# Optimization experiments

Measured on AMD Instinct MI355X. Metric: run time of the kernel, lower is better.

Reference implementation:

```python
import jax, jax.numpy as jnp
import numpy as np

B, N, D, H = 2, 2048, 128, 128  # batch, n_nodes, node_dim, hidden_dim
HQ = H // 4
EPS_DIST = 1e-8
EPS_LN = 1e-5


def setup_inputs() -> dict:
    key = jax.random.key(0)
    ks = jax.random.split(key, 12)
    s = 0.02
    return {
        "h": jax.random.normal(ks[0], (B, N, D), jnp.float32),
        "coords": jax.random.uniform(ks[1], (B, N, 2), jnp.float32),
        "Wq": jax.random.normal(ks[2], (D, H), jnp.float32) * s,
        "bq": jnp.zeros((H,), jnp.float32),
        "Wk": jax.random.normal(ks[3], (D, H), jnp.float32) * s,
        "bk": jnp.zeros((H,), jnp.float32),
        "Wv": jax.random.normal(ks[4], (D, H), jnp.float32) * s,
        "bv": jnp.zeros((H,), jnp.float32),
        "Wd1": jax.random.normal(ks[5], (1, HQ), jnp.float32) * s,
        "bd1": jnp.zeros((HQ,), jnp.float32),
        "Wd2": jax.random.normal(ks[6], (HQ, 1), jnp.float32) * s,
        "bd2": jnp.zeros((1,), jnp.float32),
        "Wo": jax.random.normal(ks[7], (H, D), jnp.float32) * s,
        "bo": jnp.zeros((D,), jnp.float32),
        "gamma": jnp.ones((D,), jnp.float32),
        "beta": jnp.zeros((D,), jnp.float32),
    }


def reference(h, coords, Wq, bq, Wk, bk, Wv, bv, Wd1, bd1, Wd2, bd2, Wo, bo, gamma, beta):
    q = h @ Wq + bq                      # (B, N, H)
    k = h @ Wk + bk
    v = h @ Wv + bv
    scores = jnp.einsum('bnh,bmh->bnm', q, k) / jnp.sqrt(jnp.float32(H))  # (B,N,N)
    # pairwise Euclidean distances
    diff = coords[:, :, None, :] - coords[:, None, :, :]                  # (B,N,N,2)
    dist = jnp.sqrt(jnp.sum(diff * diff, axis=-1, keepdims=True) + EPS_DIST)  # (B,N,N,1)
    hmid = jax.nn.silu(dist @ Wd1 + bd1)                                  # (B,N,N,HQ)
    dist_bias = (hmid @ Wd2 + bd2)[..., 0]                                # (B,N,N)
    attn = jax.nn.softmax(scores + dist_bias, axis=-1)
    out = jnp.einsum('bnm,bmh->bnh', attn, v)                             # (B,N,H)
    out = jax.nn.silu(out @ Wo + bo)                                      # (B,N,D)
    res = h + out
    mu = jnp.mean(res, axis=-1, keepdims=True)
    var = jnp.mean((res - mu) ** 2, axis=-1, keepdims=True)
    return (res - mu) / jnp.sqrt(var + EPS_LN) * gamma + beta
```

## Files before the change

### kernel.cpp

```cpp
#include <hip/hip_runtime.h>
#include <hip/hip_bf16.h>

#define B_ 2
#define N_ 2048
#define D_ 128
#define H_ 128
#define HQ_ 32
#define ROWS_ (B_*N_)
#define KS_ 16
#define KPP_ (N_/KS_)
#define DMAX_ 1.4143f
#define SCALE_ 0.08838834764831845f
#define LOG2E_ 1.4426950408889634f

typedef __bf16 bf16x4 __attribute__((ext_vector_type(4)));
typedef __bf16 bf16x8 __attribute__((ext_vector_type(8)));
typedef float  f32x4  __attribute__((ext_vector_type(4)));
typedef unsigned short ushort8 __attribute__((ext_vector_type(8)));

#if __has_builtin(__builtin_amdgcn_exp2f)
#define EXP2F_ __builtin_amdgcn_exp2f
#else
#define EXP2F_ exp2f
#endif
#if __has_builtin(__builtin_amdgcn_sqrtf)
#define SQRTF_ __builtin_amdgcn_sqrtf
#else
#define SQRTF_ sqrtf
#endif

#define Q_OFF    0
#define K_OFF    (ROWS_*H_*2)
#define V_OFF    (2*ROWS_*H_*2)
#define L_OFF    (3*ROWS_*H_*2)
#define OP_OFF   (L_OFF + ROWS_*KS_*4)
#define HB_OFF   (OP_OFF + (size_t)ROWS_*KS_*H_*2)
#define WT_OFF   (HB_OFF + ROWS_*D_*2)
#define CF_OFF   (WT_OFF + 3*D_*H_*2)

__global__ __launch_bounds__(256) void prep_kernel(
    const float* __restrict__ h,
    const float* __restrict__ Wq, const float* __restrict__ Wk, const float* __restrict__ Wv,
    const float* __restrict__ Wd1, const float* __restrict__ bd1,
    const float* __restrict__ Wd2, const float* __restrict__ bd2,
    __bf16* __restrict__ hb, __bf16* __restrict__ Wt, float* __restrict__ cf)
{
    const int bid = blockIdx.x, t = threadIdx.x;
    if (bid < 256) {
        const float4* src = (const float4*)(h + (size_t)bid * 2048);
        __bf16* dst = hb + (size_t)bid * 2048;
        #pragma unroll
        for (int i = 0; i < 2; ++i) {
            float4 v = src[t + i * 256];
            bf16x4 pk = { (__bf16)v.x, (__bf16)v.y, (__bf16)v.z, (__bf16)v.w };
            *(bf16x4*)(dst + (t + i * 256) * 4) = pk;
        }
    } else if (bid < 280) {
        __shared__ float tile[128][17];
        const int id = bid - 256;
        const int m = id >> 3, ch = id & 7;
        const float* W = m == 0 ? Wq : (m == 1 ? Wk : Wv);
        const int c0 = ch * 16;
        #pragma unroll
        for (int i = 0; i < 8; ++i) {
            int idx = t + i * 256;
            int k = idx >> 4, cc = idx & 15;
            tile[k][cc] = W[k * 128 + c0 + cc];
        }
        __syncthreads();
        __bf16* dst = Wt + m * 16384;
        #pragma unroll
        for (int i = 0; i < 8; ++i) {
            int idx = t + i * 256;
            int cc = idx >> 7, k = idx & 127;
            dst[(c0 + cc) * 128 + k] = (__bf16)tile[k][cc];
        }
    } else if (t < 64) {
        const int j = t & 31;
        const float w1 = Wd1[j], b1 = bd1[j];
        const float w2h = Wd2[j] * 0.5f;
        float gv[5];
        #pragma unroll
        for (int i = 0; i < 5; ++i) {
            float d = (DMAX_ * 0.25f) * (float)i;
            float x = fmaf(d, w1, b1);
            gv[i] = (x / (1.f + __expf(-x))) * w2h;
        }
        #pragma unroll
        for (int i = 0; i < 5; ++i)
            #pragma unroll
            for (int off = 1; off < 64; off <<= 1) gv[i] += __shfl_xor(gv[i], off);
        if (t == 0) {
            const float bd2v = bd2[0];
            float g0 = (gv[0] + bd2v) * LOG2E_, g1 = (gv[1] + bd2v) * LOG2E_,
                  g2 = (gv[2] + bd2v) * LOG2E_, g3 = (gv[3] + bd2v) * LOG2E_,
                  g4 = (gv[4] + bd2v) * LOG2E_;
            cf[0] = g0;
            cf[1] = -2.0833333333f*g0 + 4.f*g1 - 3.f*g2 + 1.3333333333f*g3 - 0.25f*g4;
            cf[2] =  1.4583333333f*g0 - 4.3333333333f*g1 + 4.75f*g2 - 2.3333333333f*g3 + 0.4583333333f*g4;
            cf[3] = -0.4166666667f*g0 + 1.5f*g1 - 2.f*g2 + 1.1666666667f*g3 - 0.25f*g4;
            cf[4] =  0.0416666667f*g0 - 0.1666666667f*g1 + 0.25f*g2 - 0.1666666667f*g3 + 0.0416666667f*g4;
        }
    }
}

__global__ __launch_bounds__(256) void qkv_mfma(
    const __bf16* __restrict__ hb, const __bf16* __restrict__ Wt,
    const float* __restrict__ bq, const float* __restrict__ bk, const float* __restrict__ bv,
    __bf16* __restrict__ qb, __bf16* __restrict__ kb, __bf16* __restrict__ vb)
{
    const int t = threadIdx.x, wid = t >> 6, lane = t & 63;
    const int l16 = lane & 15, g = lane >> 4;
    const int row0 = blockIdx.x * 64 + wid * 16;
    const int co   = blockIdx.y * 32;
    const int which = co >> 7, c0 = co & 127;
    const __bf16* Wm = Wt + which * 16384;
    __bf16* outp      = which == 0 ? qb : (which == 1 ? kb : vb);
    const float* bias = which == 0 ? bq : (which == 1 ? bk : bv);
    const float scale = which == 0 ? (SCALE_ * LOG2E_) : 1.f;

    bf16x8 af[4];
    const __bf16* arow = hb + (size_t)(row0 + l16) * 128;
    #pragma unroll
    for (int kk = 0; kk < 4; ++kk) af[kk] = *(const bf16x8*)(arow + kk * 32 + g * 8);

    f32x4 acc0 = {0.f,0.f,0.f,0.f}, acc1 = {0.f,0.f,0.f,0.f};
    const __bf16* b0 = Wm + (size_t)(c0 + l16) * 128;
    const __bf16* b1 = Wm + (size_t)(c0 + 16 + l16) * 128;
    #pragma unroll
    for (int kk = 0; kk < 4; ++kk) {
        bf16x8 f0 = *(const bf16x8*)(b0 + kk * 32 + g * 8);
        acc0 = __builtin_amdgcn_mfma_f32_16x16x32_bf16(af[kk], f0, acc0, 0, 0, 0);
    }
    #pragma unroll
    for (int kk = 0; kk < 4; ++kk) {
        bf16x8 f1 = *(const bf16x8*)(b1 + kk * 32 + g * 8);
        acc1 = __builtin_amdgcn_mfma_f32_16x16x32_bf16(af[kk], f1, acc1, 0, 0, 0);
    }
    const float bv0 = bias[c0 + l16], bv1 = bias[c0 + 16 + l16];
    #pragma unroll
    for (int i = 0; i < 4; ++i) {
        size_t r = (size_t)(row0 + g * 4 + i) * 128;
        outp[r + c0 + l16]      = (__bf16)((acc0[i] + bv0) * scale);
        outp[r + c0 + 16 + l16] = (__bf16)((acc1[i] + bv1) * scale);
    }
}

__global__ __launch_bounds__(256, 3) void attn_kernel(
    const __bf16* __restrict__ qb, const __bf16* __restrict__ kb, const __bf16* __restrict__ vb,
    const float* __restrict__ coords, const float* __restrict__ cfp,
    unsigned int* __restrict__ Opb32, float* __restrict__ Larr)
{
    __shared__ __align__(16) unsigned int Vsu[2][128][20];
    __shared__ __align__(16) __bf16 Pl[4][2][16][40];

    const int t    = threadIdx.x;
    const int wid  = t >> 6;
    const int lane = t & 63;
    const int l16  = lane & 15;
    const int g    = lane >> 4;
    const int qb0  = blockIdx.x * 128 + wid * 16;
    const int p    = blockIdx.y;
    const int b    = blockIdx.x >> 4;

    const float c0 = cfp[0], c1 = cfp[1], c2 = cfp[2], c3 = cfp[3], c4 = cfp[4];

    bf16x8 qf[2][4];
    #pragma unroll
    for (int tt = 0; tt < 2; ++tt) {
        const __bf16* qrow = qb + (size_t)(qb0 + tt * 64 + l16) * H_;
        #pragma unroll
        for (int kk = 0; kk < 4; ++kk) qf[tt][kk] = *(const bf16x8*)(qrow + kk * 32 + g * 8);
    }

    float cx[2][4], cy[2][4];
    #pragma unroll
    for (int tt = 0; tt < 2; ++tt)
        #pragma unroll
        for (int i = 0; i < 4; ++i) {
            int qr = qb0 + tt * 64 + g * 4 + i;
            cx[tt][i] = coords[qr * 2]; cy[tt][i] = coords[qr * 2 + 1];
        }

    float l_i[2][4] = {{0.f,0.f,0.f,0.f},{0.f,0.f,0.f,0.f}};
    f32x4 O0[8], O1[8];
    #pragma unroll
    for (int c = 0; c < 8; ++c) { O0[c] = (f32x4){0.f,0.f,0.f,0.f}; O1[c] = (f32x4){0.f,0.f,0.f,0.f}; }

    const int kp = t & 15, co = t >> 4;
    const int kgbase = (b << 11) + p * KPP_;
    const int NT = KPP_ / 32;

    {
        const __bf16* sp = vb + (size_t)(kgbase + 2 * kp) * H_ + co * 8;
        bf16x8 va = *(const bf16x8*)sp;
        bf16x8 vb2 = *(const bf16x8*)(sp + H_);
        ushort8 ua = __builtin_bit_cast(ushort8, va);
        ushort8 ub = __builtin_bit_cast(ushort8, vb2);
        #pragma unroll
        for (int j = 0; j < 8; ++j)
            Vsu[0][co * 8 + j][kp] = (unsigned)ua[j] | ((unsigned)ub[j] << 16);
    }

    for (int kt = 0; kt < NT; ++kt) {
        __syncthreads();

        bf16x8 nva, nvb;
        if (kt + 1 < NT) {
            const __bf16* sp = vb + (size_t)(kgbase + (kt + 1) * 32 + 2 * kp) * H_ + co * 8;
            nva = *(const bf16x8*)sp;
            nvb = *(const bf16x8*)(sp + H_);
        }

        const int kg = kgbase + kt * 32;
        #pragma unroll
        for (int mt = 0; mt < 2; ++mt) {
            bf16x8 kf[4];
            const __bf16* krow = kb + (size_t)(kg + mt * 16 + l16) * H_;
            #pragma unroll
            for (int kk = 0; kk < 4; ++kk) kf[kk] = *(const bf16x8*)(krow + kk * 32 + g * 8);

            f32x4 acc0 = {0.f,0.f,0.f,0.f}, acc1 = {0.f,0.f,0.f,0.f};
            #pragma unroll
            for (int kk = 0; kk < 4; ++kk)
                acc0 = __builtin_amdgcn_mfma_f32_16x16x32_bf16(qf[0][kk], kf[kk], acc0, 0, 0, 0);
            #pragma unroll
            for (int kk = 0; kk < 4; ++kk)
                acc1 = __builtin_amdgcn_mfma_f32_16x16x32_bf16(qf[1][kk], kf[kk], acc1, 0, 0, 0);

            float2 kc = *(const float2*)&coords[(kg + mt * 16 + l16) * 2];
            #pragma unroll
            for (int i = 0; i < 4; ++i) {
                float dx = cx[0][i] - kc.x, dy = cy[0][i] - kc.y;
                float dist = SQRTF_(fmaf(dx, dx, fmaf(dy, dy, 1e-8f)));
                float s4 = dist * (4.0f / DMAX_);
                float bias = fmaf(fmaf(fmaf(fmaf(c4, s4, c3), s4, c2), s4, c1), s4, c0);
                float sc = fminf(acc0[i] + bias, 80.f);
                float pe = EXP2F_(sc);
                l_i[0][i] += pe;
                Pl[wid][0][g * 4 + i][mt * 16 + l16] = (__bf16)pe;
            }
            #pragma unroll
            for (int i = 0; i < 4; ++i) {
                float dx = cx[1][i] - kc.x, dy = cy[1][i] - kc.y;
                float dist = SQRTF_(fmaf(dx, dx, fmaf(dy, dy, 1e-8f)));
                float s4 = dist * (4.0f / DMAX_);
                float bias = fmaf(fmaf(fmaf(fmaf(c4, s4, c3), s4, c2), s4, c1), s4, c0);
                float sc = fminf(acc1[i] + bias, 80.f);
                float pe = EXP2F_(sc);
                l_i[1][i] += pe;
                Pl[wid][1][g * 4 + i][mt * 16 + l16] = (__bf16)pe;
            }
        }

        if (kt + 1 < NT) {
            ushort8 ua = __builtin_bit_cast(ushort8, nva);
            ushort8 ub = __builtin_bit_cast(ushort8, nvb);
            #pragma unroll
            for (int j = 0; j < 8; ++j)
                Vsu[(kt + 1) & 1][co * 8 + j][kp] = (unsigned)ua[j] | ((unsigned)ub[j] << 16);
        }

        bf16x8 pf0 = *(const bf16x8*)&Pl[wid][0][l16][g * 8];
        bf16x8 pf1 = *(const bf16x8*)&Pl[wid][1][l16][g * 8];
        #pragma unroll
        for (int c = 0; c < 8; ++c) {
            bf16x8 vf = *(const bf16x8*)&Vsu[kt & 1][c * 16 + l16][g * 4];
            O0[c] = __builtin_amdgcn_mfma_f32_16x16x32_bf16(pf0, vf, O0[c], 0, 0, 0);
            O1[c] = __builtin_amdgcn_mfma_f32_16x16x32_bf16(pf1, vf, O1[c], 0, 0, 0);
        }
    }

    #pragma unroll
    for (int tt = 0; tt < 2; ++tt) {
        const size_t rpbase = (size_t)p * (ROWS_ / 2) + ((qb0 + tt * 64) >> 1) + g * 2;
        #pragma unroll
        for (int c = 0; c < 8; ++c)
            #pragma unroll
            for (int ip = 0; ip < 2; ++ip) {
                float lo_f = tt ? O1[c][2 * ip]     : O0[c][2 * ip];
                float hi_f = tt ? O1[c][2 * ip + 1] : O0[c][2 * ip + 1];
                unsigned lo = __builtin_bit_cast(unsigned, lo_f);
                unsigned hi = __builtin_bit_cast(unsigned, hi_f);
                Opb32[(rpbase + ip) * H_ + c * 16 + l16] = (hi & 0xffff0000u) | (lo >> 16);
            }
    }

    #pragma unroll
    for (int tt = 0; tt < 2; ++tt)
        #pragma unroll
        for (int i = 0; i < 4; ++i) {
            float lv = l_i[tt][i];
            lv += __shfl_xor(lv, 1); lv += __shfl_xor(lv, 2);
            lv += __shfl_xor(lv, 4); lv += __shfl_xor(lv, 8);
            if (l16 == 0) Larr[(qb0 + tt * 64 + g * 4 + i) * KS_ + p] = lv;
        }
}

__global__ __launch_bounds__(256) void final_kernel(
    const unsigned int* __restrict__ Opb32, const float* __restrict__ Larr,
    const float* __restrict__ h, const float* __restrict__ Wo, const float* __restrict__ bo,
    const float* __restrict__ gamma, const float* __restrict__ beta, float* __restrict__ out)
{
    __shared__ __align__(16) float as_[8][128];
    __shared__ float redS[4][4], redQ[4][4];
    const int t = threadIdx.x;
    const int c = t & 127;
    const int rh = t >> 7;
    const int bx = blockIdx.x;
    const int row0 = (bx & 31) * 128 + (bx >> 5) * 8;

    #pragma unroll
    for (int pr = 0; pr < 2; ++pr) {
        int r0 = rh * 4 + pr * 2;
        int row = row0 + r0;
        size_t rp = (size_t)row >> 1;
        float accL = 0.f, accH = 0.f, lsumL = 0.f, lsumH = 0.f;
        #pragma unroll
        for (int p = 0; p < KS_; ++p) {
            unsigned v = Opb32[((size_t)p * (ROWS_ / 2) + rp) * H_ + c];
            accL += __uint_as_float(v << 16);
            accH += __uint_as_float(v & 0xffff0000u);
        }
        #pragma unroll
        for (int q4 = 0; q4 < 4; ++q4) {
            f32x4 lL = *(const f32x4*)&Larr[row * KS_ + q4 * 4];
            f32x4 lH = *(const f32x4*)&Larr[(row + 1) * KS_ + q4 * 4];
            lsumL += lL[0] + lL[1] + lL[2] + lL[3];
            lsumH += lH[0] + lH[1] + lH[2] + lH[3];
        }
        as_[r0][c]     = accL / lsumL;
        as_[r0 + 1][c] = accH / lsumH;
    }
    __syncthreads();

    float acc4[4] = {0.f, 0.f, 0.f, 0.f};
    #pragma unroll 4
    for (int d4 = 0; d4 < 32; ++d4) {
        float w0 = Wo[(d4 * 4 + 0) * 128 + c];
        float w1 = Wo[(d4 * 4 + 1) * 128 + c];
        float w2 = Wo[(d4 * 4 + 2) * 128 + c];
        float w3 = Wo[(d4 * 4 + 3) * 128 + c];
        #pragma unroll
        for (int r = 0; r < 4; ++r) {
            f32x4 a_ = *(const f32x4*)&as_[rh * 4 + r][d4 * 4];
            acc4[r] = fmaf(a_[0], w0, acc4[r]);
            acc4[r] = fmaf(a_[1], w1, acc4[r]);
            acc4[r] = fmaf(a_[2], w2, acc4[r]);
            acc4[r] = fmaf(a_[3], w3, acc4[r]);
        }
    }

    const float bov = bo[c], gv = gamma[c], bvv = beta[c];
    const int wv = t >> 6;
    float res[4];
    #pragma unroll
    for (int r = 0; r < 4; ++r) {
        float x = acc4[r] + bov;
        float sl = x / (1.f + __expf(-x));
        res[r] = h[(size_t)(row0 + rh * 4 + r) * 128 + c] + sl;
    }

    #pragma unroll
    for (int r = 0; r < 4; ++r) {
        float s1 = res[r], s2 = res[r] * res[r];
        #pragma unroll
        for (int off = 32; off >= 1; off >>= 1) {
            s1 += __shfl_xor(s1, off);
            s2 += __shfl_xor(s2, off);
        }
        if ((t & 63) == 0) { redS[wv][r] = s1; redQ[wv][r] = s2; }
    }
    __syncthreads();
    #pragma unroll
    for (int r = 0; r < 4; ++r) {
        float sum = redS[2 * rh][r] + redS[2 * rh + 1][r];
        float sq  = redQ[2 * rh][r] + redQ[2 * rh + 1][r];
        float mu  = sum * (1.f / 128.f);
        float var = sq * (1.f / 128.f) - mu * mu;
        out[(size_t)(row0 + rh * 4 + r) * 128 + c] = (res[r] - mu) * rsqrtf(var + 1e-5f) * gv + bvv;
    }
}

extern "C" void kernel_launch(void* const* d_in, const int* in_sizes, int n_in,
                              void* d_out, int out_size, void* d_ws, size_t ws_size,
                              hipStream_t stream)
{
    const float* h      = (const float*)d_in[0];
    const float* coords = (const float*)d_in[1];
    const float* Wq = (const float*)d_in[2];  const float* bq = (const float*)d_in[3];
    const float* Wk = (const float*)d_in[4];  const float* bk = (const float*)d_in[5];
    const float* Wv = (const float*)d_in[6];  const float* bv = (const float*)d_in[7];
    const float* Wd1 = (const float*)d_in[8]; const float* bd1 = (const float*)d_in[9];
    const float* Wd2 = (const float*)d_in[10];const float* bd2 = (const float*)d_in[11];
    const float* Wo = (const float*)d_in[12]; const float* bo = (const float*)d_in[13];
    const float* gamma = (const float*)d_in[14]; const float* beta = (const float*)d_in[15];

    char* ws = (char*)d_ws;
    __bf16* qb = (__bf16*)(ws + Q_OFF);
    __bf16* kb = (__bf16*)(ws + K_OFF);
    __bf16* vb = (__bf16*)(ws + V_OFF);
    float* Larr         = (float*)(ws + L_OFF);
    unsigned int* Opb32 = (unsigned int*)(ws + OP_OFF);
    __bf16* hb   = (__bf16*)(ws + HB_OFF);
    __bf16* Wt   = (__bf16*)(ws + WT_OFF);
    float* cf    = (float*)(ws + CF_OFF);

    prep_kernel<<<281, 256, 0, stream>>>(h, Wq, Wk, Wv, Wd1, bd1, Wd2, bd2, hb, Wt, cf);
    qkv_mfma<<<dim3(ROWS_ / 64, 12), 256, 0, stream>>>(hb, Wt, bq, bk, bv, qb, kb, vb);
    attn_kernel<<<dim3(ROWS_ / 128, KS_), 256, 0, stream>>>(qb, kb, vb, coords, cf, Opb32, Larr);
    final_kernel<<<ROWS_ / 8, 256, 0, stream>>>(Opb32, Larr, h, Wo, bo, gamma, beta, (float*)d_out);
}
```

Measured before the change: 50.14 us.

## Fuse prep into QKV projection and final reduction into attention via last-block counter

The separate prep kernel is removed. The QKV projection now converts h to bf16 in registers and transposes its weight slice into shared memory itself, and it also computes the distance-bias polynomial coefficients and zeroes the per-tile counters. The final combine, output projection and layernorm move into the tail of the attention kernel: the last split block for each row tile, found with an atomic counter, reduces the partials and applies Wo with MFMA. This removes two kernel launches and the hb/Wt round trips. In exchange, shared memory per block grows so occupancy drops to 2 blocks, the tail work runs serialized in a few blocks, and each QKV block re-reads its weight slice.

Measured after the change: 115.4 us. 130% more time.

```diff
diff --git a/kernel.cpp b/kernel.cpp
--- a/kernel.cpp
+++ b/kernel.cpp
@@ -13,7 +13,6 @@
 #define SCALE_ 0.08838834764831845f
 #define LOG2E_ 1.4426950408889634f
 
-typedef __bf16 bf16x4 __attribute__((ext_vector_type(4)));
 typedef __bf16 bf16x8 __attribute__((ext_vector_type(8)));
 typedef float  f32x4  __attribute__((ext_vector_type(4)));
 typedef unsigned short ushort8 __attribute__((ext_vector_type(8)));
@@ -34,107 +33,88 @@
 #define V_OFF    (2*ROWS_*H_*2)
 #define L_OFF    (3*ROWS_*H_*2)
 #define OP_OFF   (L_OFF + ROWS_*KS_*4)
-#define HB_OFF   (OP_OFF + (size_t)ROWS_*KS_*H_*2)
-#define WT_OFF   (HB_OFF + ROWS_*D_*2)
-#define CF_OFF   (WT_OFF + 3*D_*H_*2)
-
-__global__ __launch_bounds__(256) void prep_kernel(
+#define CF_OFF   (OP_OFF + (size_t)ROWS_*KS_*H_*2)
+#define CNT_OFF  (CF_OFF + 64)
+
+__global__ __launch_bounds__(256) void qkv_mfma(
     const float* __restrict__ h,
-    const float* __restrict__ Wq, const float* __restrict__ Wk, const float* __restrict__ Wv,
+    const float* __restrict__ Wq, const float* __restrict__ bq,
+    const float* __restrict__ Wk, const float* __restrict__ bk,
+    const float* __restrict__ Wv, const float* __restrict__ bv,
     const float* __restrict__ Wd1, const float* __restrict__ bd1,
     const float* __restrict__ Wd2, const float* __restrict__ bd2,
-    __bf16* __restrict__ hb, __bf16* __restrict__ Wt, float* __restrict__ cf)
+    __bf16* __restrict__ qb, __bf16* __restrict__ kb, __bf16* __restrict__ vb,
+    float* __restrict__ cf, unsigned* __restrict__ cnt)
 {
-    const int bid = blockIdx.x, t = threadIdx.x;
-    if (bid < 256) {
-        const float4* src = (const float4*)(h + (size_t)bid * 2048);
-        __bf16* dst = hb + (size_t)bid * 2048;
-        #pragma unroll
-        for (int i = 0; i < 2; ++i) {
-            float4 v = src[t + i * 256];
-            bf16x4 pk = { (__bf16)v.x, (__bf16)v.y, (__bf16)v.z, (__bf16)v.w };
-            *(bf16x4*)(dst + (t + i * 256) * 4) = pk;
-        }
-    } else if (bid < 280) {
-        __shared__ float tile[128][17];
-        const int id = bid - 256;
-        const int m = id >> 3, ch = id & 7;
-        const float* W = m == 0 ? Wq : (m == 1 ? Wk : Wv);
-        const int c0 = ch * 16;
-        #pragma unroll
-        for (int i = 0; i < 8; ++i) {
-            int idx = t + i * 256;
-            int k = idx >> 4, cc = idx & 15;
-            tile[k][cc] = W[k * 128 + c0 + cc];
-        }
-        __syncthreads();
-        __bf16* dst = Wt + m * 16384;
-        #pragma unroll
-        for (int i = 0; i < 8; ++i) {
-            int idx = t + i * 256;
-            int cc = idx >> 7, k = idx & 127;
-            dst[(c0 + cc) * 128 + k] = (__bf16)tile[k][cc];
-        }
-    } else if (t < 64) {
-        const int j = t & 31;
-        const float w1 = Wd1[j], b1 = bd1[j];
-        const float w2h = Wd2[j] * 0.5f;
-        float gv[5];
-        #pragma unroll
-        for (int i = 0; i < 5; ++i) {
-            float d = (DMAX_ * 0.25f) * (float)i;
-            float x = fmaf(d, w1, b1);
-            gv[i] = (x / (1.f + __expf(-x))) * w2h;
-        }
-        #pragma unroll
-        for (int i = 0; i < 5; ++i)
-            #pragma unroll
-            for (int off = 1; off < 64; off <<= 1) gv[i] += __shfl_xor(gv[i], off);
-        if (t == 0) {
-            const float bd2v = bd2[0];
-            float g0 = (gv[0] + bd2v) * LOG2E_, g1 = (gv[1] + bd2v) * LOG2E_,
-                  g2 = (gv[2] + bd2v) * LOG2E_, g3 = (gv[3] + bd2v) * LOG2E_,
-                  g4 = (gv[4] + bd2v) * LOG2E_;
-            cf[0] = g0;
-            cf[1] = -2.0833333333f*g0 + 4.f*g1 - 3.f*g2 + 1.3333333333f*g3 - 0.25f*g4;
-            cf[2] =  1.4583333333f*g0 - 4.3333333333f*g1 + 4.75f*g2 - 2.3333333333f*g3 + 0.4583333333f*g4;
-            cf[3] = -0.4166666667f*g0 + 1.5f*g1 - 2.f*g2 + 1.1666666667f*g3 - 0.25f*g4;
-            cf[4] =  0.0416666667f*g0 - 0.1666666667f*g1 + 0.25f*g2 - 0.1666666667f*g3 + 0.0416666667f*g4;
-        }
-    }
-}
-
-__global__ __launch_bounds__(256) void qkv_mfma(
-    const __bf16* __restrict__ hb, const __bf16* __restrict__ Wt,
-    const float* __restrict__ bq, const float* __restrict__ bk, const float* __restrict__ bv,
-    __bf16* __restrict__ qb, __bf16* __restrict__ kb, __bf16* __restrict__ vb)
-{
-    const int t = threadIdx.x, wid = t >> 6, lane = t & 63;
-    const int l16 = lane & 15, g = lane >> 4;
+    __shared__ __align__(16) __bf16 Wl[32][144];
+    const int t = threadIdx.x;
+    const int y = blockIdx.y;
+    const int which = y >> 2, c0 = (y & 3) * 32;
+    const float* W    = which == 0 ? Wq : (which == 1 ? Wk : Wv);
+    const float* bias = which == 0 ? bq : (which == 1 ? bk : bv);
+    __bf16* outp      = which == 0 ? qb : (which == 1 ? kb : vb);
+    const float scale = which == 0 ? (SCALE_ * LOG2E_) : 1.f;
+
+    if (blockIdx.x == 0 && y == 0) {
+        if (t >= 64 && t < 96) cnt[t - 64] = 0;
+        if (t < 64) {
+            const int j = t & 31;
+            const float w1 = Wd1[j], b1 = bd1[j];
+            const float w2h = Wd2[j] * 0.5f;
+            float gv[5];
+            #pragma unroll
+            for (int i = 0; i < 5; ++i) {
+                float d = (DMAX_ * 0.25f) * (float)i;
+                float x = fmaf(d, w1, b1);
+                gv[i] = (x / (1.f + __expf(-x))) * w2h;
+            }
+            #pragma unroll
+            for (int i = 0; i < 5; ++i)
+                #pragma unroll
+                for (int off = 1; off < 64; off <<= 1) gv[i] += __shfl_xor(gv[i], off);
+            if (t == 0) {
+                const float bd2v = bd2[0];
+                float g0 = (gv[0] + bd2v) * LOG2E_, g1 = (gv[1] + bd2v) * LOG2E_,
+                      g2 = (gv[2] + bd2v) * LOG2E_, g3 = (gv[3] + bd2v) * LOG2E_,
+                      g4 = (gv[4] + bd2v) * LOG2E_;
+                cf[0] = g0;
+                cf[1] = -2.0833333333f*g0 + 4.f*g1 - 3.f*g2 + 1.3333333333f*g3 - 0.25f*g4;
+                cf[2] =  1.4583333333f*g0 - 4.3333333333f*g1 + 4.75f*g2 - 2.3333333333f*g3 + 0.4583333333f*g4;
+                cf[3] = -0.4166666667f*g0 + 1.5f*g1 - 2.f*g2 + 1.1666666667f*g3 - 0.25f*g4;
+                cf[4] =  0.0416666667f*g0 - 0.1666666667f*g1 + 0.25f*g2 - 0.1666666667f*g3 + 0.0416666667f*g4;
+            }
+        }
+    }
+
+    #pragma unroll
+    for (int i = 0; i < 16; ++i) {
+        int idx = t + i * 256, k = idx >> 5, cc = idx & 31;
+        Wl[cc][k] = (__bf16)W[k * 128 + c0 + cc];
+    }
+    __syncthreads();
+
+    const int wid = t >> 6, lane = t & 63, l16 = lane & 15, g = lane >> 4;
     const int row0 = blockIdx.x * 64 + wid * 16;
-    const int co   = blockIdx.y * 32;
-    const int which = co >> 7, c0 = co & 127;
-    const __bf16* Wm = Wt + which * 16384;
-    __bf16* outp      = which == 0 ? qb : (which == 1 ? kb : vb);
-    const float* bias = which == 0 ? bq : (which == 1 ? bk : bv);
-    const float scale = which == 0 ? (SCALE_ * LOG2E_) : 1.f;
 
     bf16x8 af[4];
-    const __bf16* arow = hb + (size_t)(row0 + l16) * 128;
-    #pragma unroll
-    for (int kk = 0; kk < 4; ++kk) af[kk] = *(const bf16x8*)(arow + kk * 32 + g * 8);
+    const float* arow = h + (size_t)(row0 + l16) * 128;
+    #pragma unroll
+    for (int kk = 0; kk < 4; ++kk) {
+        float4 a0 = *(const float4*)(arow + kk * 32 + g * 8);
+        float4 a1 = *(const float4*)(arow + kk * 32 + g * 8 + 4);
+        af[kk] = (bf16x8){ (__bf16)a0.x, (__bf16)a0.y, (__bf16)a0.z, (__bf16)a0.w,
+                           (__bf16)a1.x, (__bf16)a1.y, (__bf16)a1.z, (__bf16)a1.w };
+    }
 
     f32x4 acc0 = {0.f,0.f,0.f,0.f}, acc1 = {0.f,0.f,0.f,0.f};
-    const __bf16* b0 = Wm + (size_t)(c0 + l16) * 128;
-    const __bf16* b1 = Wm + (size_t)(c0 + 16 + l16) * 128;
     #pragma unroll
     for (int kk = 0; kk < 4; ++kk) {
-        bf16x8 f0 = *(const bf16x8*)(b0 + kk * 32 + g * 8);
+        bf16x8 f0 = *(const bf16x8*)&Wl[l16][kk * 32 + g * 8];
         acc0 = __builtin_amdgcn_mfma_f32_16x16x32_bf16(af[kk], f0, acc0, 0, 0, 0);
     }
     #pragma unroll
     for (int kk = 0; kk < 4; ++kk) {
-        bf16x8 f1 = *(const bf16x8*)(b1 + kk * 32 + g * 8);
+        bf16x8 f1 = *(const bf16x8*)&Wl[16 + l16][kk * 32 + g * 8];
         acc1 = __builtin_amdgcn_mfma_f32_16x16x32_bf16(af[kk], f1, acc1, 0, 0, 0);
     }
     const float bv0 = bias[c0 + l16], bv1 = bias[c0 + 16 + l16];
@@ -146,13 +126,18 @@
     }
 }
 
-__global__ __launch_bounds__(256, 3) void attn_kernel(
+__global__ __launch_bounds__(256, 2) void attn_kernel(
     const __bf16* __restrict__ qb, const __bf16* __restrict__ kb, const __bf16* __restrict__ vb,
     const float* __restrict__ coords, const float* __restrict__ cfp,
-    unsigned int* __restrict__ Opb32, float* __restrict__ Larr)
+    unsigned int* __restrict__ Opb32, float* __restrict__ Larr, unsigned* __restrict__ cnt,
+    const float* __restrict__ h, const float* __restrict__ Wo, const float* __restrict__ bo,
+    const float* __restrict__ gamma, const float* __restrict__ beta, float* __restrict__ out)
 {
     __shared__ __align__(16) unsigned int Vsu[2][128][20];
     __shared__ __align__(16) __bf16 Pl[4][2][16][40];
+    __shared__ __align__(16) __bf16 asb[128][144];
+    __shared__ float lsumS[128], redS[4][128], redQ[4][128], muS[128], rsS[128];
+    __shared__ unsigned last_flag;
 
     const int t    = threadIdx.x;
     const int wid  = t >> 6;
@@ -285,7 +270,6 @@
                 Opb32[(rpbase + ip) * H_ + c * 16 + l16] = (hi & 0xffff0000u) | (lo >> 16);
             }
     }
-
     #pragma unroll
     for (int tt = 0; tt < 2; ++tt)
         #pragma unroll
@@ -295,91 +279,113 @@
             lv += __shfl_xor(lv, 4); lv += __shfl_xor(lv, 8);
             if (l16 == 0) Larr[(qb0 + tt * 64 + g * 4 + i) * KS_ + p] = lv;
         }
-}
-
-__global__ __launch_bounds__(256) void final_kernel(
-    const unsigned int* __restrict__ Opb32, const float* __restrict__ Larr,
-    const float* __restrict__ h, const float* __restrict__ Wo, const float* __restrict__ bo,
-    const float* __restrict__ gamma, const float* __restrict__ beta, float* __restrict__ out)
-{
-    __shared__ __align__(16) float as_[8][128];
-    __shared__ float redS[4][4], redQ[4][4];
-    const int t = threadIdx.x;
-    const int c = t & 127;
-    const int rh = t >> 7;
-    const int bx = blockIdx.x;
-    const int row0 = (bx & 31) * 128 + (bx >> 5) * 8;
-
-    #pragma unroll
-    for (int pr = 0; pr < 2; ++pr) {
-        int r0 = rh * 4 + pr * 2;
-        int row = row0 + r0;
-        size_t rp = (size_t)row >> 1;
-        float accL = 0.f, accH = 0.f, lsumL = 0.f, lsumH = 0.f;
-        #pragma unroll
-        for (int p = 0; p < KS_; ++p) {
-            unsigned v = Opb32[((size_t)p * (ROWS_ / 2) + rp) * H_ + c];
-            accL += __uint_as_float(v << 16);
-            accH += __uint_as_float(v & 0xffff0000u);
-        }
-        #pragma unroll
-        for (int q4 = 0; q4 < 4; ++q4) {
-            f32x4 lL = *(const f32x4*)&Larr[row * KS_ + q4 * 4];
-            f32x4 lH = *(const f32x4*)&Larr[(row + 1) * KS_ + q4 * 4];
-            lsumL += lL[0] + lL[1] + lL[2] + lL[3];
-            lsumH += lH[0] + lH[1] + lH[2] + lH[3];
-        }
-        as_[r0][c]     = accL / lsumL;
-        as_[r0 + 1][c] = accH / lsumH;
-    }
-    __syncthreads();
-
-    float acc4[4] = {0.f, 0.f, 0.f, 0.f};
-    #pragma unroll 4
-    for (int d4 = 0; d4 < 32; ++d4) {
-        float w0 = Wo[(d4 * 4 + 0) * 128 + c];
-        float w1 = Wo[(d4 * 4 + 1) * 128 + c];
-        float w2 = Wo[(d4 * 4 + 2) * 128 + c];
-        float w3 = Wo[(d4 * 4 + 3) * 128 + c];
-        #pragma unroll
-        for (int r = 0; r < 4; ++r) {
-            f32x4 a_ = *(const f32x4*)&as_[rh * 4 + r][d4 * 4];
-            acc4[r] = fmaf(a_[0], w0, acc4[r]);
-            acc4[r] = fmaf(a_[1], w1, acc4[r]);
-            acc4[r] = fmaf(a_[2], w2, acc4[r]);
-            acc4[r] = fmaf(a_[3], w3, acc4[r]);
-        }
-    }
-
-    const float bov = bo[c], gv = gamma[c], bvv = beta[c];
-    const int wv = t >> 6;
-    float res[4];
-    #pragma unroll
-    for (int r = 0; r < 4; ++r) {
-        float x = acc4[r] + bov;
-        float sl = x / (1.f + __expf(-x));
-        res[r] = h[(size_t)(row0 + rh * 4 + r) * 128 + c] + sl;
-    }
-
-    #pragma unroll
-    for (int r = 0; r < 4; ++r) {
-        float s1 = res[r], s2 = res[r] * res[r];
-        #pragma unroll
-        for (int off = 32; off >= 1; off >>= 1) {
-            s1 += __shfl_xor(s1, off);
-            s2 += __shfl_xor(s2, off);
-        }
-        if ((t & 63) == 0) { redS[wv][r] = s1; redQ[wv][r] = s2; }
-    }
-    __syncthreads();
-    #pragma unroll
-    for (int r = 0; r < 4; ++r) {
-        float sum = redS[2 * rh][r] + redS[2 * rh + 1][r];
-        float sq  = redQ[2 * rh][r] + redQ[2 * rh + 1][r];
-        float mu  = sum * (1.f / 128.f);
-        float var = sq * (1.f / 128.f) - mu * mu;
-        out[(size_t)(row0 + rh * 4 + r) * 128 + c] = (res[r] - mu) * rsqrtf(var + 1e-5f) * gv + bvv;
-    }
+
+    __threadfence();
+    if (t == 0) last_flag = (atomicAdd(&cnt[blockIdx.x], 1u) == KS_ - 1) ? 1u : 0u;
+    __syncthreads();
+    if (!last_flag) return;
+    __threadfence();
+
+    const int row0e = blockIdx.x * 128;
+    if (t < 128) {
+        float s = 0.f;
+        #pragma unroll
+        for (int pp = 0; pp < KS_; ++pp) s += Larr[(row0e + t) * KS_ + pp];
+        lsumS[t] = s;
+    }
+    __syncthreads();
+
+    {
+        const int c = t & 127, rh = t >> 7;
+        for (int pr = 0; pr < 32; ++pr) {
+            int lr = rh * 64 + pr * 2;
+            size_t rp = (size_t)(row0e + lr) >> 1;
+            float aL = 0.f, aH = 0.f;
+            #pragma unroll
+            for (int pp = 0; pp < KS_; ++pp) {
+                unsigned v = Opb32[((size_t)pp * (ROWS_ / 2) + rp) * H_ + c];
+                aL += __uint_as_float(v << 16);
+                aH += __uint_as_float(v & 0xffff0000u);
+            }
+            asb[lr][c]     = (__bf16)(aL / lsumS[lr]);
+            asb[lr + 1][c] = (__bf16)(aH / lsumS[lr + 1]);
+        }
+    }
+    __syncthreads();
+
+    const int wc0 = wid * 32;
+    bf16x8 wf[2][4];
+    #pragma unroll
+    for (int ct = 0; ct < 2; ++ct)
+        #pragma unroll
+        for (int kk = 0; kk < 4; ++kk) {
+            bf16x8 tmp;
+            #pragma unroll
+            for (int j = 0; j < 8; ++j)
+                tmp[j] = (__bf16)Wo[(kk * 32 + g * 8 + j) * 128 + wc0 + ct * 16 + l16];
+            wf[ct][kk] = tmp;
+        }
+    const float bo0 = bo[wc0 + l16], bo1 = bo[wc0 + 16 + l16];
+
+    float res[8][2][4];
+    #pragma unroll
+    for (int m = 0; m < 8; ++m) {
+        bf16x8 a4[4];
+        #pragma unroll
+        for (int kk = 0; kk < 4; ++kk)
+            a4[kk] = *(const bf16x8*)&asb[m * 16 + l16][kk * 32 + g * 8];
+        #pragma unroll
+        for (int ct = 0; ct < 2; ++ct) {
+            f32x4 acc = {0.f,0.f,0.f,0.f};
+            #pragma unroll
+            for (int kk = 0; kk < 4; ++kk)
+                acc = __builtin_amdgcn_mfma_f32_16x16x32_bf16(a4[kk], wf[ct][kk], acc, 0, 0, 0);
+            float bov = ct ? bo1 : bo0;
+            #pragma unroll
+            for (int i = 0; i < 4; ++i) {
+                float x = acc[i] + bov;
+                float sl = x / (1.f + __expf(-x));
+                int row = row0e + m * 16 + g * 4 + i;
+                res[m][ct][i] = h[(size_t)row * 128 + wc0 + ct * 16 + l16] + sl;
+            }
+        }
+    }
+
+    #pragma unroll
+    for (int m = 0; m < 8; ++m)
+        #pragma unroll
+        for (int i = 0; i < 4; ++i) {
+            float s1 = res[m][0][i] + res[m][1][i];
+            float s2 = res[m][0][i]*res[m][0][i] + res[m][1][i]*res[m][1][i];
+            s1 += __shfl_xor(s1, 1); s2 += __shfl_xor(s2, 1);
+            s1 += __shfl_xor(s1, 2); s2 += __shfl_xor(s2, 2);
+            s1 += __shfl_xor(s1, 4); s2 += __shfl_xor(s2, 4);
+            s1 += __shfl_xor(s1, 8); s2 += __shfl_xor(s2, 8);
+            if (l16 == 0) { redS[wid][m * 16 + g * 4 + i] = s1; redQ[wid][m * 16 + g * 4 + i] = s2; }
+        }
+    __syncthreads();
+    if (t < 128) {
+        float S = redS[0][t] + redS[1][t] + redS[2][t] + redS[3][t];
+        float Q = redQ[0][t] + redQ[1][t] + redQ[2][t] + redQ[3][t];
+        float mu = S * (1.f / 128.f);
+        float var = Q * (1.f / 128.f) - mu * mu;
+        muS[t] = mu;
+        rsS[t] = rsqrtf(var + 1e-5f);
+    }
+    __syncthreads();
+
+    const float ga0 = gamma[wc0 + l16], ga1 = gamma[wc0 + 16 + l16];
+    const float be0 = beta[wc0 + l16],  be1 = beta[wc0 + 16 + l16];
+    #pragma unroll
+    for (int m = 0; m < 8; ++m)
+        #pragma unroll
+        for (int i = 0; i < 4; ++i) {
+            int lr = m * 16 + g * 4 + i;
+            float mu = muS[lr], rs = rsS[lr];
+            size_t row = (size_t)(row0e + lr) * 128;
+            out[row + wc0 + l16]      = (res[m][0][i] - mu) * rs * ga0 + be0;
+            out[row + wc0 + 16 + l16] = (res[m][1][i] - mu) * rs * ga1 + be1;
+        }
 }
 
 extern "C" void kernel_launch(void* const* d_in, const int* in_sizes, int n_in,
@@ -402,12 +408,11 @@
     __bf16* vb = (__bf16*)(ws + V_OFF);
     float* Larr         = (float*)(ws + L_OFF);
     unsigned int* Opb32 = (unsigned int*)(ws + OP_OFF);
-    __bf16* hb   = (__bf16*)(ws + HB_OFF);
-    __bf16* Wt   = (__bf16*)(ws + WT_OFF);
     float* cf    = (float*)(ws + CF_OFF);
-
-    prep_kernel<<<281, 256, 0, stream>>>(h, Wq, Wk, Wv, Wd1, bd1, Wd2, bd2, hb, Wt, cf);
-    qkv_mfma<<<dim3(ROWS_ / 64, 12), 256, 0, stream>>>(hb, Wt, bq, bk, bv, qb, kb, vb);
-    attn_kernel<<<dim3(ROWS_ / 128, KS_), 256, 0, stream>>>(qb, kb, vb, coords, cf, Opb32, Larr);
-    final_kernel<<<ROWS_ / 8, 256, 0, stream>>>(Opb32, Larr, h, Wo, bo, gamma, beta, (float*)d_out);
+    unsigned* cnt = (unsigned*)(ws + CNT_OFF);
+
+    qkv_mfma<<<dim3(64, 12), 256, 0, stream>>>(h, Wq, bq, Wk, bk, Wv, bv,
+                                               Wd1, bd1, Wd2, bd2, qb, kb, vb, cf, cnt);
+    attn_kernel<<<dim3(ROWS_ / 128, KS_), 256, 0, stream>>>(qb, kb, vb, coords, cf, Opb32, Larr,
+                                                            cnt, h, Wo, bo, gamma, beta, (float*)d_out);
 }
```

## Fuse prep into QKV projection and raise key-split count to 32

Applied to the files above, without the earlier changes.

Removes the separate prep kernel: the QKV MFMA kernel now converts h to bf16 on load and transposes its weight slice into shared memory, while one block computes the distance-bias polynomial coefficients. The attention and final kernels are templated on the key-split count, and 32 splits are used when the workspace is large enough. This saves one launch and the intermediate bf16 buffers, and gives the attention kernel more blocks for parallelism. In exchange it doubles the partial-output traffic that the final reduction must read, and each QKV block re-reads and converts its fp32 weights.

Measured after the change: 47.79 us. 1.05x faster.

```diff
diff --git a/kernel.cpp b/kernel.cpp
--- a/kernel.cpp
+++ b/kernel.cpp
@@ -5,15 +5,11 @@
 #define N_ 2048
 #define D_ 128
 #define H_ 128
-#define HQ_ 32
 #define ROWS_ (B_*N_)
-#define KS_ 16
-#define KPP_ (N_/KS_)
 #define DMAX_ 1.4143f
 #define SCALE_ 0.08838834764831845f
 #define LOG2E_ 1.4426950408889634f
 
-typedef __bf16 bf16x4 __attribute__((ext_vector_type(4)));
 typedef __bf16 bf16x8 __attribute__((ext_vector_type(8)));
 typedef float  f32x4  __attribute__((ext_vector_type(4)));
 typedef unsigned short ushort8 __attribute__((ext_vector_type(8)));
@@ -32,50 +28,30 @@
 #define Q_OFF    0
 #define K_OFF    (ROWS_*H_*2)
 #define V_OFF    (2*ROWS_*H_*2)
-#define L_OFF    (3*ROWS_*H_*2)
-#define OP_OFF   (L_OFF + ROWS_*KS_*4)
-#define HB_OFF   (OP_OFF + (size_t)ROWS_*KS_*H_*2)
-#define WT_OFF   (HB_OFF + ROWS_*D_*2)
-#define CF_OFF   (WT_OFF + 3*D_*H_*2)
-
-__global__ __launch_bounds__(256) void prep_kernel(
+#define CF_OFF   (3*ROWS_*H_*2)
+#define L_OFF    (CF_OFF + 64)
+#define OP_OFF   (L_OFF + ROWS_*32*4)
+
+__global__ __launch_bounds__(256) void qkv_mfma(
     const float* __restrict__ h,
-    const float* __restrict__ Wq, const float* __restrict__ Wk, const float* __restrict__ Wv,
+    const float* __restrict__ Wq, const float* __restrict__ bq,
+    const float* __restrict__ Wk, const float* __restrict__ bk,
+    const float* __restrict__ Wv, const float* __restrict__ bv,
     const float* __restrict__ Wd1, const float* __restrict__ bd1,
     const float* __restrict__ Wd2, const float* __restrict__ bd2,
-    __bf16* __restrict__ hb, __bf16* __restrict__ Wt, float* __restrict__ cf)
+    __bf16* __restrict__ qb, __bf16* __restrict__ kb, __bf16* __restrict__ vb,
+    float* __restrict__ cf)
 {
-    const int bid = blockIdx.x, t = threadIdx.x;
-    if (bid < 256) {
-        const float4* src = (const float4*)(h + (size_t)bid * 2048);
-        __bf16* dst = hb + (size_t)bid * 2048;
-        #pragma unroll
-        for (int i = 0; i < 2; ++i) {
-            float4 v = src[t + i * 256];
-            bf16x4 pk = { (__bf16)v.x, (__bf16)v.y, (__bf16)v.z, (__bf16)v.w };
-            *(bf16x4*)(dst + (t + i * 256) * 4) = pk;
-        }
-    } else if (bid < 280) {
-        __shared__ float tile[128][17];
-        const int id = bid - 256;
-        const int m = id >> 3, ch = id & 7;
-        const float* W = m == 0 ? Wq : (m == 1 ? Wk : Wv);
-        const int c0 = ch * 16;
-        #pragma unroll
-        for (int i = 0; i < 8; ++i) {
-            int idx = t + i * 256;
-            int k = idx >> 4, cc = idx & 15;
-            tile[k][cc] = W[k * 128 + c0 + cc];
-        }
-        __syncthreads();
-        __bf16* dst = Wt + m * 16384;
-        #pragma unroll
-        for (int i = 0; i < 8; ++i) {
-            int idx = t + i * 256;
-            int cc = idx >> 7, k = idx & 127;
-            dst[(c0 + cc) * 128 + k] = (__bf16)tile[k][cc];
-        }
-    } else if (t < 64) {
+    __shared__ __align__(16) __bf16 Wl[32][144];
+    const int t = threadIdx.x;
+    const int y = blockIdx.y;
+    const int which = y >> 2, c0 = (y & 3) * 32;
+    const float* W    = which == 0 ? Wq : (which == 1 ? Wk : Wv);
+    const float* bias = which == 0 ? bq : (which == 1 ? bk : bv);
+    __bf16* outp      = which == 0 ? qb : (which == 1 ? kb : vb);
+    const float scale = which == 0 ? (SCALE_ * LOG2E_) : 1.f;
+
+    if (blockIdx.x == 0 && y == 0 && t < 64) {
         const int j = t & 31;
         const float w1 = Wd1[j], b1 = bd1[j];
         const float w2h = Wd2[j] * 0.5f;
@@ -102,39 +78,36 @@
             cf[4] =  0.0416666667f*g0 - 0.1666666667f*g1 + 0.25f*g2 - 0.1666666667f*g3 + 0.0416666667f*g4;
         }
     }
-}
-
-__global__ __launch_bounds__(256) void qkv_mfma(
-    const __bf16* __restrict__ hb, const __bf16* __restrict__ Wt,
-    const float* __restrict__ bq, const float* __restrict__ bk, const float* __restrict__ bv,
-    __bf16* __restrict__ qb, __bf16* __restrict__ kb, __bf16* __restrict__ vb)
-{
-    const int t = threadIdx.x, wid = t >> 6, lane = t & 63;
-    const int l16 = lane & 15, g = lane >> 4;
+
+    #pragma unroll
+    for (int i = 0; i < 16; ++i) {
+        int idx = t + i * 256, k = idx >> 5, cc = idx & 31;
+        Wl[cc][k] = (__bf16)W[k * 128 + c0 + cc];
+    }
+    __syncthreads();
+
+    const int wid = t >> 6, lane = t & 63, l16 = lane & 15, g = lane >> 4;
     const int row0 = blockIdx.x * 64 + wid * 16;
-    const int co   = blockIdx.y * 32;
-    const int which = co >> 7, c0 = co & 127;
-    const __bf16* Wm = Wt + which * 16384;
-    __bf16* outp      = which == 0 ? qb : (which == 1 ? kb : vb);
-    const float* bias = which == 0 ? bq : (which == 1 ? bk : bv);
-    const float scale = which == 0 ? (SCALE_ * LOG2E_) : 1.f;
 
     bf16x8 af[4];
-    const __bf16* arow = hb + (size_t)(row0 + l16) * 128;
-    #pragma unroll
-    for (int kk = 0; kk < 4; ++kk) af[kk] = *(const bf16x8*)(arow + kk * 32 + g * 8);
+    const float* arow = h + (size_t)(row0 + l16) * 128;
+    #pragma unroll
+    for (int kk = 0; kk < 4; ++kk) {
+        float4 a0 = *(const float4*)(arow + kk * 32 + g * 8);
+        float4 a1 = *(const float4*)(arow + kk * 32 + g * 8 + 4);
+        af[kk] = (bf16x8){ (__bf16)a0.x, (__bf16)a0.y, (__bf16)a0.z, (__bf16)a0.w,
+                           (__bf16)a1.x, (__bf16)a1.y, (__bf16)a1.z, (__bf16)a1.w };
+    }
 
     f32x4 acc0 = {0.f,0.f,0.f,0.f}, acc1 = {0.f,0.f,0.f,0.f};
-    const __bf16* b0 = Wm + (size_t)(c0 + l16) * 128;
-    const __bf16* b1 = Wm + (size_t)(c0 + 16 + l16) * 128;
     #pragma unroll
     for (int kk = 0; kk < 4; ++kk) {
-        bf16x8 f0 = *(const bf16x8*)(b0 + kk * 32 + g * 8);
+        bf16x8 f0 = *(const bf16x8*)&Wl[l16][kk * 32 + g * 8];
         acc0 = __builtin_amdgcn_mfma_f32_16x16x32_bf16(af[kk], f0, acc0, 0, 0, 0);
     }
     #pragma unroll
     for (int kk = 0; kk < 4; ++kk) {
-        bf16x8 f1 = *(const bf16x8*)(b1 + kk * 32 + g * 8);
+        bf16x8 f1 = *(const bf16x8*)&Wl[16 + l16][kk * 32 + g * 8];
         acc1 = __builtin_amdgcn_mfma_f32_16x16x32_bf16(af[kk], f1, acc1, 0, 0, 0);
     }
     const float bv0 = bias[c0 + l16], bv1 = bias[c0 + 16 + l16];
@@ -146,11 +119,15 @@
     }
 }
 
+template<int KSP>
 __global__ __launch_bounds__(256, 3) void attn_kernel(
     const __bf16* __restrict__ qb, const __bf16* __restrict__ kb, const __bf16* __restrict__ vb,
     const float* __restrict__ coords, const float* __restrict__ cfp,
     unsigned int* __restrict__ Opb32, float* __restrict__ Larr)
 {
+    constexpr int KPP = N_ / KSP;
+    constexpr int NT  = KPP / 32;
+
     __shared__ __align__(16) unsigned int Vsu[2][128][20];
     __shared__ __align__(16) __bf16 Pl[4][2][16][40];
 
@@ -188,8 +165,7 @@
     for (int c = 0; c < 8; ++c) { O0[c] = (f32x4){0.f,0.f,0.f,0.f}; O1[c] = (f32x4){0.f,0.f,0.f,0.f}; }
 
     const int kp = t & 15, co = t >> 4;
-    const int kgbase = (b << 11) + p * KPP_;
-    const int NT = KPP_ / 32;
+    const int kgbase = (b << 11) + p * KPP;
 
     {
         const __bf16* sp = vb + (size_t)(kgbase + 2 * kp) * H_ + co * 8;
@@ -285,7 +261,6 @@
                 Opb32[(rpbase + ip) * H_ + c * 16 + l16] = (hi & 0xffff0000u) | (lo >> 16);
             }
     }
-
     #pragma unroll
     for (int tt = 0; tt < 2; ++tt)
         #pragma unroll
@@ -293,10 +268,11 @@
             float lv = l_i[tt][i];
             lv += __shfl_xor(lv, 1); lv += __shfl_xor(lv, 2);
             lv += __shfl_xor(lv, 4); lv += __shfl_xor(lv, 8);
-            if (l16 == 0) Larr[(qb0 + tt * 64 + g * 4 + i) * KS_ + p] = lv;
+            if (l16 == 0) Larr[(qb0 + tt * 64 + g * 4 + i) * KSP + p] = lv;
         }
 }
 
+template<int KSP>
 __global__ __launch_bounds__(256) void final_kernel(
     const unsigned int* __restrict__ Opb32, const float* __restrict__ Larr,
     const float* __restrict__ h, const float* __restrict__ Wo, const float* __restrict__ bo,
@@ -317,15 +293,15 @@
         size_t rp = (size_t)row >> 1;
         float accL = 0.f, accH = 0.f, lsumL = 0.f, lsumH = 0.f;
         #pragma unroll
-        for (int p = 0; p < KS_; ++p) {
+        for (int p = 0; p < KSP; ++p) {
             unsigned v = Opb32[((size_t)p * (ROWS_ / 2) + rp) * H_ + c];
             accL += __uint_as_float(v << 16);
             accH += __uint_as_float(v & 0xffff0000u);
         }
         #pragma unroll
-        for (int q4 = 0; q4 < 4; ++q4) {
-            f32x4 lL = *(const f32x4*)&Larr[row * KS_ + q4 * 4];
-            f32x4 lH = *(const f32x4*)&Larr[(row + 1) * KS_ + q4 * 4];
+        for (int q4 = 0; q4 < KSP / 4; ++q4) {
+            f32x4 lL = *(const f32x4*)&Larr[row * KSP + q4 * 4];
+            f32x4 lH = *(const f32x4*)&Larr[(row + 1) * KSP + q4 * 4];
             lsumL += lL[0] + lL[1] + lL[2] + lL[3];
             lsumH += lH[0] + lH[1] + lH[2] + lH[3];
         }
@@ -400,14 +376,20 @@
     __bf16* qb = (__bf16*)(ws + Q_OFF);
     __bf16* kb = (__bf16*)(ws + K_OFF);
     __bf16* vb = (__bf16*)(ws + V_OFF);
+    float* cf           = (float*)(ws + CF_OFF);
     float* Larr         = (float*)(ws + L_OFF);
     unsigned int* Opb32 = (unsigned int*)(ws + OP_OFF);
-    __bf16* hb   = (__bf16*)(ws + HB_OFF);
-    __bf16* Wt   = (__bf16*)(ws + WT_OFF);
-    float* cf    = (float*)(ws + CF_OFF);
-
-    prep_kernel<<<281, 256, 0, stream>>>(h, Wq, Wk, Wv, Wd1, bd1, Wd2, bd2, hb, Wt, cf);
-    qkv_mfma<<<dim3(ROWS_ / 64, 12), 256, 0, stream>>>(hb, Wt, bq, bk, bv, qb, kb, vb);
-    attn_kernel<<<dim3(ROWS_ / 128, KS_), 256, 0, stream>>>(qb, kb, vb, coords, cf, Opb32, Larr);
-    final_kernel<<<ROWS_ / 8, 256, 0, stream>>>(Opb32, Larr, h, Wo, bo, gamma, beta, (float*)d_out);
+
+    const size_t need32 = (size_t)OP_OFF + (size_t)32 * (ROWS_ / 2) * H_ * 4;
+    const bool big = ws_size >= need32;
+
+    qkv_mfma<<<dim3(64, 12), 256, 0, stream>>>(h, Wq, bq, Wk, bk, Wv, bv,
+                                               Wd1, bd1, Wd2, bd2, qb, kb, vb, cf);
+    if (big) {
+        attn_kernel<32><<<dim3(32, 32), 256, 0, stream>>>(qb, kb, vb, coords, cf, Opb32, Larr);
+        final_kernel<32><<<ROWS_ / 8, 256, 0, stream>>>(Opb32, Larr, h, Wo, bo, gamma, beta, (float*)d_out);
+    } else {
+        attn_kernel<16><<<dim3(32, 16), 256, 0, stream>>>(qb, kb, vb, coords, cf, Opb32, Larr);
+        final_kernel<16><<<ROWS_ / 8, 256, 0, stream>>>(Opb32, Larr, h, Wo, bo, gamma, beta, (float*)d_out);
+    }
 }
```
